# Kernel optimization log

Measured on AMD Instinct MI355X. Metric: run time of the kernel, lower is better.

## Reference

```python
import jax, jax.numpy as jnp
import numpy as np

L, B, N, IN, H, ATTN, RED, OUT = 3, 8, 512, 64, 128, 32, 32, 3


def setup_inputs() -> dict:
    key = jax.random.key(0)
    ks = jax.random.split(key, 34)
    def rn(i, shape, s=0.05):
        return jax.random.normal(ks[i], shape, dtype=jnp.float32) * s
    inp = {
        "X": rn(0, (B, N, IN), 1.0),
        # sparse binary adjacency (avg degree ~10) and denser clique graph
        "A": (jax.random.uniform(ks[1], (B, N, N)) < 0.02).astype(jnp.float32),
        "Ac": (jax.random.uniform(ks[2], (B, N, N)) < 0.05).astype(jnp.float32),
        # topo embedding
        "embed_w": rn(3, (H, IN)), "embed_b": jnp.zeros((H,), jnp.float32),
        "topo_eps": jnp.zeros((1,), jnp.float32),
        "topo_w": rn(4, (H, H)), "topo_b": jnp.zeros((H,), jnp.float32),
        "theta": rn(5, (H, 2)),
        # per-layer dual GIN (index 0: A, index 1: Ac)
        "gin_eps": jnp.zeros((L, 2, 1), jnp.float32),
        "gin_w": rn(6, (L, 2, H, H)), "gin_b": jnp.zeros((L, 2, H), jnp.float32),
        # per-layer flexible attention
        "wo": rn(7, (L, ATTN, H)), "w1": rn(8, (L, ATTN, H)),
        "wphi": rn(9, (L, ATTN)),
        "wy_w": rn(10, (L, H, H)), "wy_b": jnp.zeros((L, H), jnp.float32),
        "we_w": rn(11, (L, H, ATTN)), "we_b": jnp.zeros((L, H), jnp.float32),
        # per-layer SE block
        "lin1_w": rn(12, (L, RED, H)), "lin1_b": jnp.zeros((L, RED), jnp.float32),
        "lin2_w": rn(13, (L, H, RED)), "lin2_b": jnp.zeros((L, H), jnp.float32),
        "mlp_w": rn(14, (L, H, H)), "mlp_b": jnp.zeros((L, H), jnp.float32),
        # node head
        "head1_w": rn(15, (H // 2, H)), "head1_b": jnp.zeros((H // 2,), jnp.float32),
        "head2_w": rn(16, (OUT, H // 2)), "head2_b": jnp.zeros((OUT,), jnp.float32),
    }
    return inp


def _lin(x, w, b=None):
    y = x @ w.T
    return y if b is None else y + b


def _gin(x, a, eps, w, b):
    # (1+eps)*X + A@X, then Linear, then ReLU
    return jax.nn.relu(_lin((1.0 + eps) * x + a @ x, w, b))


def _forward(X, A, Ac, embed_w, embed_b, topo_eps, topo_w, topo_b, theta,
             gin_eps, gin_w, gin_b, wo, w1, wphi, wy_w, wy_b, we_w, we_b,
             lin1_w, lin1_b, lin2_w, lin2_b, mlp_w, mlp_b,
             head1_w, head1_b, head2_w, head2_b):
    # TopoPositionalEmbedding (shared GIN on both graphs)
    Xh = _lin(X, embed_w, embed_b)                      # (B,N,H)
    hA = _gin(Xh, A, topo_eps[0], topo_w, topo_b)
    hAC = _gin(Xh, Ac, topo_eps[0], topo_w, topo_b)
    Xp = Xh + jnp.tanh(hA * theta[:, 0]) + jnp.tanh(hAC * theta[:, 1])

    for l in range(L):
        # dual GIN
        XA = _gin(Xp, A, gin_eps[l, 0, 0], gin_w[l, 0], gin_b[l, 0])
        XAC = _gin(Xp, Ac, gin_eps[l, 1, 0], gin_w[l, 1], gin_b[l, 1])
        # GRIT-style flexible attention
        ho = Xp @ wo[l].T                               # (B,N,ATTN)
        h1 = Xp @ w1[l].T
        e = jnp.tanh(ho[:, :, None, :] + h1[:, None, :, :])   # (B,N,N,ATTN)
        alpha = jax.nn.softmax(e @ wphi[l], axis=-1)    # (B,N,N)
        Xy = _lin(Xp, wy_w[l], wy_b[l])                 # (B,N,H)
        # sum_j alpha_ij * We(e_ij) == We(sum_j alpha_ij * e_ij) since We is affine
        # and sum_j alpha_ij == 1 (avoids the (B,N,N,H) intermediate)
        ctx = jnp.einsum('bij,bijd->bid', alpha, e)     # (B,N,ATTN)
        Xatt = alpha @ Xy + _lin(ctx, we_w[l], we_b[l])
        Xbar = XA + XAC + Xatt
        # SE gating
        y1 = jax.nn.relu(_lin(Xbar.sum(axis=1), lin1_w[l], lin1_b[l]))
        y2 = jax.nn.sigmoid(_lin(y1, lin2_w[l], lin2_b[l]))
        Xp = _lin(Xbar * y2[:, None, :], mlp_w[l], mlp_b[l])

    h = jax.nn.relu(_lin(Xp, head1_w, head1_b))
    return _lin(h, head2_w, head2_b)                    # (B,N,OUT)


def reference(X, A, Ac, embed_w, embed_b, topo_eps, topo_w, topo_b, theta,
              gin_eps, gin_w, gin_b, wo, w1, wphi, wy_w, wy_b, we_w, we_b,
              lin1_w, lin1_b, lin2_w, lin2_b, mlp_w, mlp_b,
              head1_w, head1_b, head2_w, head2_b):
    return _forward(X, A, Ac, embed_w, embed_b, topo_eps, topo_w, topo_b, theta,
                    gin_eps, gin_w, gin_b, wo, w1, wphi, wy_w, wy_b, we_w, we_b,
                    lin1_w, lin1_b, lin2_w, lin2_b, mlp_w, mlp_b,
                    head1_w, head1_b, head2_w, head2_b)
```

## Files before the change

### kernel.cpp

```cpp
#include <hip/hip_runtime.h>

#define Bc 8
#define Nc 512
#define INc 64
#define Hc 128
#define Atc 32
#define REDc 32
#define OUTc 3
#define Lc 3
#define MNc (Bc * Nc)

__device__ __forceinline__ float tanh_fast(float x) {
    float e = __expf(2.f * x);
    return 1.f - 2.f * __builtin_amdgcn_rcpf(e + 1.f);
}

template <int TM, int K, int ACT>
__global__ __launch_bounds__(256) void gemm256(
        const float* __restrict__ X, const float* __restrict__ W,
        const float* __restrict__ bias, float* __restrict__ Y,
        const float* __restrict__ scale) {
    constexpr int RPG = TM / 2;
    __shared__ float xs[TM * K];
    int m0 = blockIdx.x * TM;
    int t = threadIdx.x;
    const float* sc = scale ? scale + (size_t)(m0 >> 9) * K : nullptr;
    for (int idx4 = t; idx4 < TM * K / 4; idx4 += 256) {
        float4 v = ((const float4*)(X + (size_t)m0 * K))[idx4];
        if (sc) {
            int base = idx4 * 4;
            v.x *= sc[base & (K - 1)]; v.y *= sc[(base + 1) & (K - 1)];
            v.z *= sc[(base + 2) & (K - 1)]; v.w *= sc[(base + 3) & (K - 1)];
        }
        ((float4*)xs)[idx4] = v;
    }
    __syncthreads();
    int n = t & 127;
    int grp = t >> 7;
    float bv = bias ? bias[n] : 0.f;
    float acc[RPG];
#pragma unroll
    for (int r = 0; r < RPG; ++r) acc[r] = bv;
    const float* w = W + (size_t)n * K;
    for (int k = 0; k < K; k += 4) {
        float4 wv = *(const float4*)(w + k);
#pragma unroll
        for (int r = 0; r < RPG; ++r) {
            float4 xv = *(const float4*)(xs + (grp * RPG + r) * K + k);
            acc[r] = fmaf(xv.x, wv.x, acc[r]); acc[r] = fmaf(xv.y, wv.y, acc[r]);
            acc[r] = fmaf(xv.z, wv.z, acc[r]); acc[r] = fmaf(xv.w, wv.w, acc[r]);
        }
    }
#pragma unroll
    for (int r = 0; r < RPG; ++r) {
        float v = acc[r];
        if (ACT) v = fmaxf(v, 0.f);
        Y[(size_t)(m0 + grp * RPG + r) * 128 + n] = v;
    }
}

__global__ __launch_bounds__(128) void spmm2(
        const float* __restrict__ A, const float* __restrict__ Acg,
        const float* __restrict__ X, const float* __restrict__ eA,
        const float* __restrict__ eC, float* __restrict__ T1, float* __restrict__ T2) {
    int bi = blockIdx.x;
    int b = bi >> 9;
    int h = threadIdx.x;
    __shared__ int idxA[Nc], idxC[Nc];
    __shared__ int cntA, cntC;
    if (h == 0) { cntA = 0; cntC = 0; }
    __syncthreads();
    {
        float4 a4 = ((const float4*)(A + (size_t)bi * Nc))[h];
        if (a4.x != 0.f) idxA[atomicAdd(&cntA, 1)] = 4 * h;
        if (a4.y != 0.f) idxA[atomicAdd(&cntA, 1)] = 4 * h + 1;
        if (a4.z != 0.f) idxA[atomicAdd(&cntA, 1)] = 4 * h + 2;
        if (a4.w != 0.f) idxA[atomicAdd(&cntA, 1)] = 4 * h + 3;
        float4 c4 = ((const float4*)(Acg + (size_t)bi * Nc))[h];
        if (c4.x != 0.f) idxC[atomicAdd(&cntC, 1)] = 4 * h;
        if (c4.y != 0.f) idxC[atomicAdd(&cntC, 1)] = 4 * h + 1;
        if (c4.z != 0.f) idxC[atomicAdd(&cntC, 1)] = 4 * h + 2;
        if (c4.w != 0.f) idxC[atomicAdd(&cntC, 1)] = 4 * h + 3;
    }
    __syncthreads();
    int nA = cntA, nC = cntC;
    const float* Xb = X + (size_t)b * Nc * Hc;
    float a1 = 0.f, a2 = 0.f;
    for (int q = 0; q < nA; ++q) a1 += Xb[(size_t)idxA[q] * Hc + h];
    for (int q = 0; q < nC; ++q) a2 += Xb[(size_t)idxC[q] * Hc + h];
    size_t o = (size_t)bi * Hc + h;
    float xv = X[o];
    T1[o] = (1.f + eA[0]) * xv + a1;
    T2[o] = (1.f + eC[0]) * xv + a2;
}

__global__ __launch_bounds__(256) void gemm2_topo(
        const float* __restrict__ T1, const float* __restrict__ T2,
        const float* __restrict__ W, const float* __restrict__ bias,
        const float* __restrict__ Xh, const float* __restrict__ theta,
        float* __restrict__ Xp) {
    __shared__ float xs1[8 * Hc], xs2[8 * Hc];
    int m0 = blockIdx.x * 8;
    int t = threadIdx.x;
    for (int idx4 = t; idx4 < 8 * Hc / 4; idx4 += 256) {
        ((float4*)xs1)[idx4] = ((const float4*)(T1 + (size_t)m0 * Hc))[idx4];
        ((float4*)xs2)[idx4] = ((const float4*)(T2 + (size_t)m0 * Hc))[idx4];
    }
    __syncthreads();
    int n = t & 127, grp = t >> 7;
    float bv = bias[n];
    float ac1[4], ac2[4];
#pragma unroll
    for (int r = 0; r < 4; ++r) { ac1[r] = bv; ac2[r] = bv; }
    const float* w = W + (size_t)n * Hc;
    for (int k = 0; k < Hc; k += 4) {
        float4 wv = *(const float4*)(w + k);
#pragma unroll
        for (int r = 0; r < 4; ++r) {
            float4 x1 = *(const float4*)(xs1 + (grp * 4 + r) * Hc + k);
            float4 x2 = *(const float4*)(xs2 + (grp * 4 + r) * Hc + k);
            ac1[r] = fmaf(x1.x, wv.x, ac1[r]); ac1[r] = fmaf(x1.y, wv.y, ac1[r]);
            ac1[r] = fmaf(x1.z, wv.z, ac1[r]); ac1[r] = fmaf(x1.w, wv.w, ac1[r]);
            ac2[r] = fmaf(x2.x, wv.x, ac2[r]); ac2[r] = fmaf(x2.y, wv.y, ac2[r]);
            ac2[r] = fmaf(x2.z, wv.z, ac2[r]); ac2[r] = fmaf(x2.w, wv.w, ac2[r]);
        }
    }
    float th0 = theta[2 * n], th1 = theta[2 * n + 1];
#pragma unroll
    for (int r = 0; r < 4; ++r) {
        size_t o = (size_t)(m0 + grp * 4 + r) * Hc + n;
        float g1 = fmaxf(ac1[r], 0.f), g2 = fmaxf(ac2[r], 0.f);
        Xp[o] = Xh[o] + tanh_fast(g1 * th0) + tanh_fast(g2 * th1);
    }
}

__global__ __launch_bounds__(256) void layer_gemms(
        const float* __restrict__ T1, const float* __restrict__ T2,
        const float* __restrict__ W1, const float* __restrict__ b1,
        const float* __restrict__ W2, const float* __restrict__ b2,
        const float* __restrict__ Xp, const float* __restrict__ wy_w,
        const float* __restrict__ wy_b, const float* __restrict__ wo,
        const float* __restrict__ w1a, float* __restrict__ GS,
        float* __restrict__ Xy, float* __restrict__ hov, float* __restrict__ h1v) {
    __shared__ float xs1[8 * Hc], xs2[8 * Hc], xs[8 * Hc];
    int m0 = blockIdx.x * 8;
    int t = threadIdx.x;
    for (int idx4 = t; idx4 < 8 * Hc / 4; idx4 += 256) {
        ((float4*)xs1)[idx4] = ((const float4*)(T1 + (size_t)m0 * Hc))[idx4];
        ((float4*)xs2)[idx4] = ((const float4*)(T2 + (size_t)m0 * Hc))[idx4];
        ((float4*)xs)[idx4]  = ((const float4*)(Xp + (size_t)m0 * Hc))[idx4];
    }
    __syncthreads();
    int n = t & 127, grp = t >> 7;
    {
        float ac1[4], ac2[4];
        float bv1 = b1[n], bv2 = b2[n];
#pragma unroll
        for (int r = 0; r < 4; ++r) { ac1[r] = bv1; ac2[r] = bv2; }
        const float* w1 = W1 + (size_t)n * Hc;
        const float* w2 = W2 + (size_t)n * Hc;
        for (int k = 0; k < Hc; k += 4) {
            float4 wv1 = *(const float4*)(w1 + k);
            float4 wv2 = *(const float4*)(w2 + k);
#pragma unroll
            for (int r = 0; r < 4; ++r) {
                float4 x1 = *(const float4*)(xs1 + (grp * 4 + r) * Hc + k);
                float4 x2 = *(const float4*)(xs2 + (grp * 4 + r) * Hc + k);
                ac1[r] = fmaf(x1.x, wv1.x, ac1[r]); ac1[r] = fmaf(x1.y, wv1.y, ac1[r]);
                ac1[r] = fmaf(x1.z, wv1.z, ac1[r]); ac1[r] = fmaf(x1.w, wv1.w, ac1[r]);
                ac2[r] = fmaf(x2.x, wv2.x, ac2[r]); ac2[r] = fmaf(x2.y, wv2.y, ac2[r]);
                ac2[r] = fmaf(x2.z, wv2.z, ac2[r]); ac2[r] = fmaf(x2.w, wv2.w, ac2[r]);
            }
        }
#pragma unroll
        for (int r = 0; r < 4; ++r) {
            size_t o = (size_t)(m0 + grp * 4 + r) * Hc + n;
            GS[o] = fmaxf(ac1[r], 0.f) + fmaxf(ac2[r], 0.f);
        }
    }
    {
        float bv = wy_b[n];
        float acc[4];
#pragma unroll
        for (int r = 0; r < 4; ++r) acc[r] = bv;
        const float* w = wy_w + (size_t)n * Hc;
        for (int k = 0; k < Hc; k += 4) {
            float4 wv = *(const float4*)(w + k);
#pragma unroll
            for (int r = 0; r < 4; ++r) {
                float4 xv = *(const float4*)(xs + (grp * 4 + r) * Hc + k);
                acc[r] = fmaf(xv.x, wv.x, acc[r]); acc[r] = fmaf(xv.y, wv.y, acc[r]);
                acc[r] = fmaf(xv.z, wv.z, acc[r]); acc[r] = fmaf(xv.w, wv.w, acc[r]);
            }
        }
#pragma unroll
        for (int r = 0; r < 4; ++r)
            Xy[(size_t)(m0 + grp * 4 + r) * Hc + n] = acc[r];
    }
    {
        int n2 = t & 63, g2 = t >> 6;
        const float* w = (n2 < 32) ? (wo + (size_t)n2 * Hc) : (w1a + (size_t)(n2 - 32) * Hc);
        float acc[2] = {0.f, 0.f};
        for (int k = 0; k < Hc; k += 4) {
            float4 wv = *(const float4*)(w + k);
#pragma unroll
            for (int r = 0; r < 2; ++r) {
                float4 xv = *(const float4*)(xs + (g2 * 2 + r) * Hc + k);
                acc[r] = fmaf(xv.x, wv.x, acc[r]); acc[r] = fmaf(xv.y, wv.y, acc[r]);
                acc[r] = fmaf(xv.z, wv.z, acc[r]); acc[r] = fmaf(xv.w, wv.w, acc[r]);
            }
        }
#pragma unroll
        for (int r = 0; r < 2; ++r) {
            int m = m0 + g2 * 2 + r;
            float v = tanh_fast(acc[r]);
            if (n2 < 32) hov[(size_t)m * Atc + n2] = v;
            else h1v[(size_t)m * Atc + (n2 - 32)] = v;
        }
    }
}

__global__ __launch_bounds__(256, 4) void attn_part(
        const float* __restrict__ ta, const float* __restrict__ tb,
        const float* __restrict__ wphi, const float* __restrict__ Xy,
        float* __restrict__ Pp, float* __restrict__ ctxp, float* __restrict__ wsp) {
    int blk = blockIdx.x;
    int b = blk >> 8;
    int r6 = (blk >> 2) & 63;
    int js = blk & 3;
    int i0 = r6 * 8;
    int t = threadIdx.x;
    __shared__ float als[8 * 128];
    __shared__ float4 red4[1024];
    __shared__ float tas[8 * 32];
    tas[t] = ta[((size_t)b * Nc + i0) * 32 + t];
    __syncthreads();
    {
        int i = t >> 5;
        int kq = t & 3;
        int jl = (t >> 2) & 7;
        float4 wp0 = ((const float4*)wphi)[kq * 2];
        float4 wp1 = ((const float4*)wphi)[kq * 2 + 1];
        float4 ta0 = *(const float4*)(tas + i * 32 + kq * 8);
        float4 ta1 = *(const float4*)(tas + i * 32 + kq * 8 + 4);
        const float* tbb = tb + ((size_t)b * Nc + js * 128) * 32;
        const float4* p = (const float4*)(tbb + (size_t)jl * 32 + kq * 8);
        float4 c0a = p[0], c0b = p[1];
        float4 c1a = p[64], c1b = p[65];
        float ca[8];
#pragma unroll
        for (int q = 0; q < 8; ++q) ca[q] = 0.f;
        float wsum = 0.f;
#pragma unroll 4
        for (int jj = 0; jj < 16; ++jj) {
            float4 ha = c0a, hb = c0b;
            c0a = c1a; c0b = c1b;
            if (jj < 14) { c1a = p[(jj + 2) * 64]; c1b = p[(jj + 2) * 64 + 1]; }
            float e0 = (ta0.x + ha.x) * __builtin_amdgcn_rcpf(fmaf(ta0.x, ha.x, 1.f));
            float e1 = (ta0.y + ha.y) * __builtin_amdgcn_rcpf(fmaf(ta0.y, ha.y, 1.f));
            float e2 = (ta0.z + ha.z) * __builtin_amdgcn_rcpf(fmaf(ta0.z, ha.z, 1.f));
            float e3 = (ta0.w + ha.w) * __builtin_amdgcn_rcpf(fmaf(ta0.w, ha.w, 1.f));
            float e4 = (ta1.x + hb.x) * __builtin_amdgcn_rcpf(fmaf(ta1.x, hb.x, 1.f));
            float e5 = (ta1.y + hb.y) * __builtin_amdgcn_rcpf(fmaf(ta1.y, hb.y, 1.f));
            float e6 = (ta1.z + hb.z) * __builtin_amdgcn_rcpf(fmaf(ta1.z, hb.z, 1.f));
            float e7 = (ta1.w + hb.w) * __builtin_amdgcn_rcpf(fmaf(ta1.w, hb.w, 1.f));
            float s01 = fmaf(e1, wp0.y, e0 * wp0.x);
            float s23 = fmaf(e3, wp0.w, e2 * wp0.z);
            float s45 = fmaf(e5, wp1.y, e4 * wp1.x);
            float s67 = fmaf(e7, wp1.w, e6 * wp1.z);
            float sc = (s01 + s23) + (s45 + s67);
            sc += __shfl_xor(sc, 1);
            sc += __shfl_xor(sc, 2);
            float w = __expf(sc);
            if (kq == 0) als[i * 128 + jj * 8 + jl] = w;
            wsum += w;
            ca[0] = fmaf(w, e0, ca[0]);
            ca[1] = fmaf(w, e1, ca[1]);
            ca[2] = fmaf(w, e2, ca[2]);
            ca[3] = fmaf(w, e3, ca[3]);
            ca[4] = fmaf(w, e4, ca[4]);
            ca[5] = fmaf(w, e5, ca[5]);
            ca[6] = fmaf(w, e6, ca[6]);
            ca[7] = fmaf(w, e7, ca[7]);
        }
#pragma unroll
        for (int o = 16; o > 0; o >>= 1) wsum += __shfl_xor(wsum, o);
        if ((t & 31) == 0) wsp[(size_t)js * MNc + (size_t)b * Nc + i0 + i] = wsum;
#pragma unroll
        for (int q = 0; q < 8; ++q) {
            ca[q] += __shfl_xor(ca[q], 4);
            ca[q] += __shfl_xor(ca[q], 8);
            ca[q] += __shfl_xor(ca[q], 16);
        }
        if (jl == 0) {
            float* cp = ctxp + ((size_t)js * MNc + (size_t)b * Nc + i0 + i) * 32 + kq * 8;
#pragma unroll
            for (int q = 0; q < 8; ++q) cp[q] = ca[q];
        }
    }
    __syncthreads();
    {
        int h4 = t & 31, jg = t >> 5;
        const float* xp = Xy + (((size_t)b * Nc + js * 128) + jg * 16) * Hc + h4 * 4;
        float* Pb = Pp + (size_t)js * MNc * Hc;
        float4 acc[8];
#pragma unroll
        for (int r = 0; r < 8; ++r) acc[r] = make_float4(0.f, 0.f, 0.f, 0.f);
        float4 xc = *(const float4*)(xp);
        float4 xn = *(const float4*)(xp + Hc);
#pragma unroll 4
        for (int jq = 0; jq < 16; ++jq) {
            float4 x = xc;
            xc = xn;
            if (jq < 14) xn = *(const float4*)(xp + (jq + 2) * Hc);
            int j = jg * 16 + jq;
#pragma unroll
            for (int r = 0; r < 8; ++r) {
                float av = als[r * 128 + j];
                acc[r].x = fmaf(av, x.x, acc[r].x);
                acc[r].y = fmaf(av, x.y, acc[r].y);
                acc[r].z = fmaf(av, x.z, acc[r].z);
                acc[r].w = fmaf(av, x.w, acc[r].w);
            }
        }
#pragma unroll
        for (int r = 0; r < 4; ++r) red4[jg * 128 + r * 32 + h4] = acc[r];
        __syncthreads();
        if (t < 128) {
            int ii = t >> 5, hq = t & 31;
            float4 s = red4[ii * 32 + hq];
#pragma unroll
            for (int gq = 1; gq < 8; ++gq) {
                float4 p = red4[gq * 128 + ii * 32 + hq];
                s.x += p.x; s.y += p.y; s.z += p.z; s.w += p.w;
            }
            *(float4*)(Pb + ((size_t)b * Nc + i0 + ii) * Hc + hq * 4) = s;
        }
        __syncthreads();
#pragma unroll
        for (int r = 0; r < 4; ++r) red4[jg * 128 + r * 32 + h4] = acc[4 + r];
        __syncthreads();
        if (t < 128) {
            int ii = t >> 5, hq = t & 31;
            float4 s = red4[ii * 32 + hq];
#pragma unroll
            for (int gq = 1; gq < 8; ++gq) {
                float4 p = red4[gq * 128 + ii * 32 + hq];
                s.x += p.x; s.y += p.y; s.z += p.z; s.w += p.w;
            }
            *(float4*)(Pb + ((size_t)b * Nc + i0 + 4 + ii) * Hc + hq * 4) = s;
        }
    }
}

__global__ __launch_bounds__(256) void combine_se(
        const float* __restrict__ Pp, const float* __restrict__ ctxp,
        const float* __restrict__ wsp, const float* __restrict__ we_w,
        const float* __restrict__ we_b, const float* __restrict__ GS,
        float* __restrict__ Xbar, float* __restrict__ part) {
    int blk = blockIdx.x;
    int m0 = blk * 8;
    int t = threadIdx.x;
    __shared__ float ctxs[8 * 32];
    __shared__ float sinv[8];
    __shared__ float4 sred[256];
    if (t < 8) {
        float ws = 0.f;
#pragma unroll
        for (int s = 0; s < 4; ++s) ws += wsp[(size_t)s * MNc + m0 + t];
        sinv[t] = 4.f / ws;
    }
    {
        float c = 0.f;
#pragma unroll
        for (int s = 0; s < 4; ++s) c += ctxp[((size_t)s * MNc + m0) * 32 + t];
        ctxs[t] = c;
    }
    __syncthreads();
    int ii = t >> 5, hq = t & 31;
    size_t o = (size_t)(m0 + ii) * Hc + hq * 4;
    float4 ps = *(const float4*)(Pp + o);
#pragma unroll
    for (int s = 1; s < 4; ++s) {
        float4 p = *(const float4*)(Pp + (size_t)s * MNc * Hc + o);
        ps.x += p.x; ps.y += p.y; ps.z += p.z; ps.w += p.w;
    }
    float si = sinv[ii];
    const float* c = ctxs + ii * 32;
    float wec[4];
#pragma unroll
    for (int ho_ = 0; ho_ < 4; ++ho_) {
        const float4* wrow = (const float4*)(we_w + (size_t)(hq * 4 + ho_) * 32);
        float sv = 0.f;
#pragma unroll
        for (int q = 0; q < 8; ++q) {
            float4 w4 = wrow[q];
            sv = fmaf(w4.x, c[4 * q], sv); sv = fmaf(w4.y, c[4 * q + 1], sv);
            sv = fmaf(w4.z, c[4 * q + 2], sv); sv = fmaf(w4.w, c[4 * q + 3], sv);
        }
        wec[ho_] = sv;
    }
    float4 wb = *(const float4*)(we_b + hq * 4);
    float4 gv = *(const float4*)(GS + o);
    float4 outv;
    outv.x = (ps.x + wec[0]) * si + wb.x + gv.x;
    outv.y = (ps.y + wec[1]) * si + wb.y + gv.y;
    outv.z = (ps.z + wec[2]) * si + wb.z + gv.z;
    outv.w = (ps.w + wec[3]) * si + wb.w + gv.w;
    *(float4*)(Xbar + o) = outv;
    sred[ii * 32 + hq] = outv;
    __syncthreads();
    if (t < 32) {
        float4 s0 = sred[t];
#pragma unroll
        for (int g = 1; g < 8; ++g) {
            float4 p = sred[g * 32 + t];
            s0.x += p.x; s0.y += p.y; s0.z += p.z; s0.w += p.w;
        }
        *(float4*)(part + (size_t)blk * Hc + t * 4) = s0;
    }
}

__global__ __launch_bounds__(128) void se_mlp(
        const float* __restrict__ part, const float* __restrict__ l1w,
        const float* __restrict__ l1b, const float* __restrict__ l2w,
        const float* __restrict__ l2b, float* __restrict__ y2) {
    int b = blockIdx.x;
    int t = threadIdx.x;
    __shared__ float s[Hc];
    __shared__ float y1s[REDc];
    const float* pb = part + (size_t)b * 64 * Hc;
    float acc = 0.f;
    for (int p = 0; p < 64; ++p) acc += pb[p * Hc + t];
    s[t] = acc;
    __syncthreads();
    if (t < REDc) {
        float a = l1b[t];
        const float* w = l1w + (size_t)t * Hc;
        for (int k = 0; k < Hc; ++k) a = fmaf(s[k], w[k], a);
        y1s[t] = fmaxf(a, 0.f);
    }
    __syncthreads();
    {
        float a = l2b[t];
        const float* w2 = l2w + (size_t)t * REDc;
#pragma unroll
        for (int k = 0; k < REDc; ++k) a = fmaf(y1s[k], w2[k], a);
        y2[(size_t)b * Hc + t] = 1.f / (1.f + __expf(-a));
    }
}

__global__ __launch_bounds__(64) void head_kernel(const float* __restrict__ Xp, const float* __restrict__ h1w,
                            const float* __restrict__ h1b, const float* __restrict__ h2w,
                            const float* __restrict__ h2b, float* __restrict__ out) {
    int m = blockIdx.x;
    int t = threadIdx.x;
    __shared__ float xs[Hc];
    __shared__ float hs[64];
    xs[t] = Xp[(size_t)m * Hc + t];
    xs[t + 64] = Xp[(size_t)m * Hc + t + 64];
    __syncthreads();
    float a = h1b[t];
    const float* w = h1w + (size_t)t * Hc;
    for (int k = 0; k < Hc; ++k) a = fmaf(xs[k], w[k], a);
    hs[t] = fmaxf(a, 0.f);
    __syncthreads();
    if (t < OUTc) {
        float o = h2b[t];
        const float* w2 = h2w + (size_t)t * 64;
#pragma unroll
        for (int k = 0; k < 64; ++k) o = fmaf(hs[k], w2[k], o);
        out[(size_t)m * OUTc + t] = o;
    }
}

extern "C" void kernel_launch(void* const* d_in, const int* in_sizes, int n_in,
                              void* d_out, int out_size, void* d_ws, size_t ws_size,
                              hipStream_t stream) {
    const float* X       = (const float*)d_in[0];
    const float* A       = (const float*)d_in[1];
    const float* Acg     = (const float*)d_in[2];
    const float* embed_w = (const float*)d_in[3];
    const float* embed_b = (const float*)d_in[4];
    const float* topo_eps= (const float*)d_in[5];
    const float* topo_w  = (const float*)d_in[6];
    const float* topo_b  = (const float*)d_in[7];
    const float* theta   = (const float*)d_in[8];
    const float* gin_eps = (const float*)d_in[9];
    const float* gin_w   = (const float*)d_in[10];
    const float* gin_b   = (const float*)d_in[11];
    const float* wo      = (const float*)d_in[12];
    const float* w1      = (const float*)d_in[13];
    const float* wphi    = (const float*)d_in[14];
    const float* wy_w    = (const float*)d_in[15];
    const float* wy_b    = (const float*)d_in[16];
    const float* we_w    = (const float*)d_in[17];
    const float* we_b    = (const float*)d_in[18];
    const float* lin1_w  = (const float*)d_in[19];
    const float* lin1_b  = (const float*)d_in[20];
    const float* lin2_w  = (const float*)d_in[21];
    const float* lin2_b  = (const float*)d_in[22];
    const float* mlp_w   = (const float*)d_in[23];
    const float* mlp_b   = (const float*)d_in[24];
    const float* head1_w = (const float*)d_in[25];
    const float* head1_b = (const float*)d_in[26];
    const float* head2_w = (const float*)d_in[27];
    const float* head2_b = (const float*)d_in[28];
    float* out = (float*)d_out;

    float* ws = (float*)d_ws;
    const int MN = Bc * Nc;
    const size_t SZ = (size_t)MN * Hc;
    float* Xh   = ws;
    float* Xp   = Xh + SZ;
    float* T1   = Xp + SZ;
    float* T2   = T1 + SZ;
    float* GS   = T2 + SZ;
    float* Xy   = GS + SZ;
    float* hov  = Xy + SZ;
    float* h1v  = hov + (size_t)MN * Atc;
    float* y2   = h1v + (size_t)MN * Atc;
    float* part = y2 + (size_t)Bc * Hc;
    float* Pp   = part + (size_t)Bc * 64 * Hc;
    float* ctxp = Pp + 4 * SZ;
    float* wsp  = ctxp + (size_t)4 * MN * Atc;
    float* Xbar = T1;

    gemm256<8, INc, 0><<<MN / 8, 256, 0, stream>>>(X, embed_w, embed_b, Xh, nullptr);
    spmm2<<<MN, 128, 0, stream>>>(A, Acg, Xh, topo_eps, topo_eps, T1, T2);
    gemm2_topo<<<MN / 8, 256, 0, stream>>>(T1, T2, topo_w, topo_b, Xh, theta, Xp);

    for (int l = 0; l < Lc; ++l) {
        spmm2<<<MN, 128, 0, stream>>>(A, Acg, Xp, gin_eps + l * 2, gin_eps + l * 2 + 1, T1, T2);
        layer_gemms<<<MN / 8, 256, 0, stream>>>(T1, T2,
            gin_w + (size_t)(l * 2 + 0) * Hc * Hc, gin_b + (size_t)(l * 2 + 0) * Hc,
            gin_w + (size_t)(l * 2 + 1) * Hc * Hc, gin_b + (size_t)(l * 2 + 1) * Hc,
            Xp, wy_w + (size_t)l * Hc * Hc, wy_b + (size_t)l * Hc,
            wo + (size_t)l * Atc * Hc, w1 + (size_t)l * Atc * Hc,
            GS, Xy, hov, h1v);
        attn_part<<<MN / 8 * 4, 256, 0, stream>>>(hov, h1v, wphi + (size_t)l * Atc, Xy,
                                                  Pp, ctxp, wsp);
        combine_se<<<MN / 8, 256, 0, stream>>>(Pp, ctxp, wsp,
                                               we_w + (size_t)l * Hc * Atc,
                                               we_b + (size_t)l * Hc, GS, Xbar, part);
        se_mlp<<<Bc, 128, 0, stream>>>(part, lin1_w + (size_t)l * REDc * Hc, lin1_b + (size_t)l * REDc,
                                       lin2_w + (size_t)l * Hc * REDc, lin2_b + (size_t)l * Hc, y2);
        gemm256<8, Hc, 0><<<MN / 8, 256, 0, stream>>>(Xbar, mlp_w + (size_t)l * Hc * Hc,
                                                      mlp_b + (size_t)l * Hc, Xp, y2);
    }
    head_kernel<<<MN, 64, 0, stream>>>(Xp, head1_w, head1_b, head2_w, head2_b, out);
}
```

Before: 444.7 us.

## Precompute CSR neighbor lists once, fuse SE MLP into MLP GEMM, batch head rows

Adjacency scanning moves into a separate build_csr kernel that runs once per call, so the four SpMM launches reuse the stored index lists instead of rescanning the dense A and Ac rows each time. The SE gating MLP is folded into the MLP GEMM kernel, which removes one launch per layer but makes every block recompute the 64-partial reduction and the small MLP. The head kernel now handles 8 rows per 256-thread block instead of one row per 64-thread block. The workspace grows by two MN×N int index arrays.

```diff
diff --git a/kernel.cpp b/kernel.cpp
--- a/kernel.cpp
+++ b/kernel.cpp
@@ -59,35 +59,50 @@
     }
 }
 
-__global__ __launch_bounds__(128) void spmm2(
+__global__ __launch_bounds__(128) void build_csr(
         const float* __restrict__ A, const float* __restrict__ Acg,
+        int* __restrict__ idxA, int* __restrict__ idxC,
+        int* __restrict__ cntA, int* __restrict__ cntC) {
+    int bi = blockIdx.x;
+    int h = threadIdx.x;
+    __shared__ int cA, cC;
+    if (h == 0) { cA = 0; cC = 0; }
+    __syncthreads();
+    int* ia = idxA + (size_t)bi * Nc;
+    int* ic = idxC + (size_t)bi * Nc;
+    {
+        float4 a4 = ((const float4*)(A + (size_t)bi * Nc))[h];
+        if (a4.x != 0.f) ia[atomicAdd(&cA, 1)] = 4 * h;
+        if (a4.y != 0.f) ia[atomicAdd(&cA, 1)] = 4 * h + 1;
+        if (a4.z != 0.f) ia[atomicAdd(&cA, 1)] = 4 * h + 2;
+        if (a4.w != 0.f) ia[atomicAdd(&cA, 1)] = 4 * h + 3;
+        float4 c4 = ((const float4*)(Acg + (size_t)bi * Nc))[h];
+        if (c4.x != 0.f) ic[atomicAdd(&cC, 1)] = 4 * h;
+        if (c4.y != 0.f) ic[atomicAdd(&cC, 1)] = 4 * h + 1;
+        if (c4.z != 0.f) ic[atomicAdd(&cC, 1)] = 4 * h + 2;
+        if (c4.w != 0.f) ic[atomicAdd(&cC, 1)] = 4 * h + 3;
+    }
+    __syncthreads();
+    if (h == 0) { cntA[bi] = cA; cntC[bi] = cC; }
+}
+
+__global__ __launch_bounds__(128) void spmm_pre(
+        const int* __restrict__ idxA, const int* __restrict__ idxC,
+        const int* __restrict__ cntA, const int* __restrict__ cntC,
         const float* __restrict__ X, const float* __restrict__ eA,
         const float* __restrict__ eC, float* __restrict__ T1, float* __restrict__ T2) {
     int bi = blockIdx.x;
     int b = bi >> 9;
     int h = threadIdx.x;
-    __shared__ int idxA[Nc], idxC[Nc];
-    __shared__ int cntA, cntC;
-    if (h == 0) { cntA = 0; cntC = 0; }
-    __syncthreads();
-    {
-        float4 a4 = ((const float4*)(A + (size_t)bi * Nc))[h];
-        if (a4.x != 0.f) idxA[atomicAdd(&cntA, 1)] = 4 * h;
-        if (a4.y != 0.f) idxA[atomicAdd(&cntA, 1)] = 4 * h + 1;
-        if (a4.z != 0.f) idxA[atomicAdd(&cntA, 1)] = 4 * h + 2;
-        if (a4.w != 0.f) idxA[atomicAdd(&cntA, 1)] = 4 * h + 3;
-        float4 c4 = ((const float4*)(Acg + (size_t)bi * Nc))[h];
-        if (c4.x != 0.f) idxC[atomicAdd(&cntC, 1)] = 4 * h;
-        if (c4.y != 0.f) idxC[atomicAdd(&cntC, 1)] = 4 * h + 1;
-        if (c4.z != 0.f) idxC[atomicAdd(&cntC, 1)] = 4 * h + 2;
-        if (c4.w != 0.f) idxC[atomicAdd(&cntC, 1)] = 4 * h + 3;
-    }
-    __syncthreads();
-    int nA = cntA, nC = cntC;
+    __shared__ int ias[Nc], ics[Nc];
+    int nA = cntA[bi], nC = cntC[bi];
+    for (int q = h; q < nA; q += 128) ias[q] = idxA[(size_t)bi * Nc + q];
+    for (int q = h; q < nC; q += 128) ics[q] = idxC[(size_t)bi * Nc + q];
+    __syncthreads();
     const float* Xb = X + (size_t)b * Nc * Hc;
     float a1 = 0.f, a2 = 0.f;
-    for (int q = 0; q < nA; ++q) a1 += Xb[(size_t)idxA[q] * Hc + h];
-    for (int q = 0; q < nC; ++q) a2 += Xb[(size_t)idxC[q] * Hc + h];
+    for (int q = 0; q < nA; ++q) a1 += Xb[(size_t)ias[q] * Hc + h];
+    for (int q = 0; q < nC; ++q) a2 += Xb[(size_t)ics[q] * Hc + h];
     size_t o = (size_t)bi * Hc + h;
     float xv = X[o];
     T1[o] = (1.f + eA[0]) * xv + a1;
@@ -421,18 +436,26 @@
     }
 }
 
-__global__ __launch_bounds__(128) void se_mlp(
-        const float* __restrict__ part, const float* __restrict__ l1w,
-        const float* __restrict__ l1b, const float* __restrict__ l2w,
-        const float* __restrict__ l2b, float* __restrict__ y2) {
-    int b = blockIdx.x;
-    int t = threadIdx.x;
+__global__ __launch_bounds__(256) void mlp_gemm(
+        const float* __restrict__ Xbar, const float* __restrict__ W,
+        const float* __restrict__ bias, const float* __restrict__ part,
+        const float* __restrict__ l1w, const float* __restrict__ l1b,
+        const float* __restrict__ l2w, const float* __restrict__ l2b,
+        float* __restrict__ Y) {
+    __shared__ float xs[8 * Hc];
     __shared__ float s[Hc];
     __shared__ float y1s[REDc];
-    const float* pb = part + (size_t)b * 64 * Hc;
-    float acc = 0.f;
-    for (int p = 0; p < 64; ++p) acc += pb[p * Hc + t];
-    s[t] = acc;
+    __shared__ float y2s[Hc];
+    int m0 = blockIdx.x * 8;
+    int b = m0 >> 9;
+    int t = threadIdx.x;
+    ((float4*)xs)[t] = ((const float4*)(Xbar + (size_t)m0 * Hc))[t];
+    if (t < 128) {
+        const float* pb = part + (size_t)b * 64 * Hc;
+        float acc = 0.f;
+        for (int p = 0; p < 64; ++p) acc += pb[p * Hc + t];
+        s[t] = acc;
+    }
     __syncthreads();
     if (t < REDc) {
         float a = l1b[t];
@@ -441,36 +464,78 @@
         y1s[t] = fmaxf(a, 0.f);
     }
     __syncthreads();
-    {
+    if (t < 128) {
         float a = l2b[t];
         const float* w2 = l2w + (size_t)t * REDc;
 #pragma unroll
         for (int k = 0; k < REDc; ++k) a = fmaf(y1s[k], w2[k], a);
-        y2[(size_t)b * Hc + t] = 1.f / (1.f + __expf(-a));
-    }
-}
-
-__global__ __launch_bounds__(64) void head_kernel(const float* __restrict__ Xp, const float* __restrict__ h1w,
-                            const float* __restrict__ h1b, const float* __restrict__ h2w,
-                            const float* __restrict__ h2b, float* __restrict__ out) {
-    int m = blockIdx.x;
+        y2s[t] = 1.f / (1.f + __expf(-a));
+    }
+    __syncthreads();
+    {
+        float4 yv = ((const float4*)y2s)[t & 31];
+        float4 v = ((float4*)xs)[t];
+        v.x *= yv.x; v.y *= yv.y; v.z *= yv.z; v.w *= yv.w;
+        ((float4*)xs)[t] = v;
+    }
+    __syncthreads();
+    int n = t & 127, grp = t >> 7;
+    float bv = bias[n];
+    float acc[4];
+#pragma unroll
+    for (int r = 0; r < 4; ++r) acc[r] = bv;
+    const float* w = W + (size_t)n * Hc;
+    for (int k = 0; k < Hc; k += 4) {
+        float4 wv = *(const float4*)(w + k);
+#pragma unroll
+        for (int r = 0; r < 4; ++r) {
+            float4 xv = *(const float4*)(xs + (grp * 4 + r) * Hc + k);
+            acc[r] = fmaf(xv.x, wv.x, acc[r]); acc[r] = fmaf(xv.y, wv.y, acc[r]);
+            acc[r] = fmaf(xv.z, wv.z, acc[r]); acc[r] = fmaf(xv.w, wv.w, acc[r]);
+        }
+    }
+#pragma unroll
+    for (int r = 0; r < 4; ++r)
+        Y[(size_t)(m0 + grp * 4 + r) * Hc + n] = acc[r];
+}
+
+__global__ __launch_bounds__(256) void head_kernel(
+        const float* __restrict__ Xp, const float* __restrict__ h1w,
+        const float* __restrict__ h1b, const float* __restrict__ h2w,
+        const float* __restrict__ h2b, float* __restrict__ out) {
+    __shared__ float xs[8 * Hc];
+    __shared__ float hs[8 * 64];
+    int m0 = blockIdx.x * 8;
     int t = threadIdx.x;
-    __shared__ float xs[Hc];
-    __shared__ float hs[64];
-    xs[t] = Xp[(size_t)m * Hc + t];
-    xs[t + 64] = Xp[(size_t)m * Hc + t + 64];
-    __syncthreads();
-    float a = h1b[t];
-    const float* w = h1w + (size_t)t * Hc;
-    for (int k = 0; k < Hc; ++k) a = fmaf(xs[k], w[k], a);
-    hs[t] = fmaxf(a, 0.f);
-    __syncthreads();
-    if (t < OUTc) {
-        float o = h2b[t];
-        const float* w2 = h2w + (size_t)t * 64;
-#pragma unroll
-        for (int k = 0; k < 64; ++k) o = fmaf(hs[k], w2[k], o);
-        out[(size_t)m * OUTc + t] = o;
+    ((float4*)xs)[t] = ((const float4*)(Xp + (size_t)m0 * Hc))[t];
+    __syncthreads();
+    {
+        int n = t & 63, grp = t >> 6;
+        float a0 = h1b[n], a1 = a0;
+        const float* w = h1w + (size_t)n * Hc;
+        const float* x0 = xs + (grp * 2) * Hc;
+        const float* x1 = xs + (grp * 2 + 1) * Hc;
+        for (int k = 0; k < Hc; k += 4) {
+            float4 wv = *(const float4*)(w + k);
+            float4 v0 = *(const float4*)(x0 + k);
+            float4 v1 = *(const float4*)(x1 + k);
+            a0 = fmaf(v0.x, wv.x, a0); a0 = fmaf(v0.y, wv.y, a0);
+            a0 = fmaf(v0.z, wv.z, a0); a0 = fmaf(v0.w, wv.w, a0);
+            a1 = fmaf(v1.x, wv.x, a1); a1 = fmaf(v1.y, wv.y, a1);
+            a1 = fmaf(v1.z, wv.z, a1); a1 = fmaf(v1.w, wv.w, a1);
+        }
+        hs[(grp * 2) * 64 + n] = fmaxf(a0, 0.f);
+        hs[(grp * 2 + 1) * 64 + n] = fmaxf(a1, 0.f);
+    }
+    __syncthreads();
+    if (t < 8 * OUTc) {
+        int m = t / OUTc, o = t - m * OUTc;
+        float a = h2b[o];
+        const float* w2 = h2w + (size_t)o * 64;
+        const float* hr = hs + m * 64;
+#pragma unroll
+        for (int k = 0; k < 64; ++k) a = fmaf(hr[k], w2[k], a);
+        out[(size_t)(m0 + m) * OUTc + o] = a;
     }
 }
 
@@ -519,19 +584,24 @@
     float* Xy   = GS + SZ;
     float* hov  = Xy + SZ;
     float* h1v  = hov + (size_t)MN * Atc;
-    float* y2   = h1v + (size_t)MN * Atc;
-    float* part = y2 + (size_t)Bc * Hc;
+    float* part = h1v + (size_t)MN * Atc;
     float* Pp   = part + (size_t)Bc * 64 * Hc;
     float* ctxp = Pp + 4 * SZ;
     float* wsp  = ctxp + (size_t)4 * MN * Atc;
+    int* idxA   = (int*)(wsp + (size_t)4 * MN);
+    int* idxC   = idxA + (size_t)MN * Nc;
+    int* cntA   = idxC + (size_t)MN * Nc;
+    int* cntC   = cntA + MN;
     float* Xbar = T1;
 
+    build_csr<<<MN, 128, 0, stream>>>(A, Acg, idxA, idxC, cntA, cntC);
     gemm256<8, INc, 0><<<MN / 8, 256, 0, stream>>>(X, embed_w, embed_b, Xh, nullptr);
-    spmm2<<<MN, 128, 0, stream>>>(A, Acg, Xh, topo_eps, topo_eps, T1, T2);
+    spmm_pre<<<MN, 128, 0, stream>>>(idxA, idxC, cntA, cntC, Xh, topo_eps, topo_eps, T1, T2);
     gemm2_topo<<<MN / 8, 256, 0, stream>>>(T1, T2, topo_w, topo_b, Xh, theta, Xp);
 
     for (int l = 0; l < Lc; ++l) {
-        spmm2<<<MN, 128, 0, stream>>>(A, Acg, Xp, gin_eps + l * 2, gin_eps + l * 2 + 1, T1, T2);
+        spmm_pre<<<MN, 128, 0, stream>>>(idxA, idxC, cntA, cntC, Xp,
+                                         gin_eps + l * 2, gin_eps + l * 2 + 1, T1, T2);
         layer_gemms<<<MN / 8, 256, 0, stream>>>(T1, T2,
             gin_w + (size_t)(l * 2 + 0) * Hc * Hc, gin_b + (size_t)(l * 2 + 0) * Hc,
             gin_w + (size_t)(l * 2 + 1) * Hc * Hc, gin_b + (size_t)(l * 2 + 1) * Hc,
@@ -543,10 +613,11 @@
         combine_se<<<MN / 8, 256, 0, stream>>>(Pp, ctxp, wsp,
                                                we_w + (size_t)l * Hc * Atc,
                                                we_b + (size_t)l * Hc, GS, Xbar, part);
-        se_mlp<<<Bc, 128, 0, stream>>>(part, lin1_w + (size_t)l * REDc * Hc, lin1_b + (size_t)l * REDc,
-                                       lin2_w + (size_t)l * Hc * REDc, lin2_b + (size_t)l * Hc, y2);
-        gemm256<8, Hc, 0><<<MN / 8, 256, 0, stream>>>(Xbar, mlp_w + (size_t)l * Hc * Hc,
-                                                      mlp_b + (size_t)l * Hc, Xp, y2);
-    }
-    head_kernel<<<MN, 64, 0, stream>>>(Xp, head1_w, head1_b, head2_w, head2_b, out);
-}
+        mlp_gemm<<<MN / 8, 256, 0, stream>>>(Xbar, mlp_w + (size_t)l * Hc * Hc,
+                                             mlp_b + (size_t)l * Hc, part,
+                                             lin1_w + (size_t)l * REDc * Hc, lin1_b + (size_t)l * REDc,
+                                             lin2_w + (size_t)l * Hc * REDc, lin2_b + (size_t)l * Hc,
+                                             Xp);
+    }
+    head_kernel<<<MN / 8, 256, 0, stream>>>(Xp, head1_w, head1_b, head2_w, head2_b, out);
+}
```

New measurement: 434.6 us, median of 2. 1.02x faster.
